# Kernel optimization log

Measured on AMD Instinct MI355X. Metric: run time of the kernel, lower is better.

## Reference

```python
import jax, jax.numpy as jnp
import numpy as np

EMBED_DIM = 1024
NUM_HEADS = 16
HEAD_DIM = EMBED_DIM // NUM_HEADS
R_QKV = 256
R_OUT = 256
B, T = 4, 2048


def setup_inputs() -> dict:
    key = jax.random.key(0)
    k1, k2, k3, k4, k5 = jax.random.split(key, 5)
    s = 0.02
    return {
        "x": jax.random.normal(k1, (B, T, EMBED_DIM), dtype=jnp.float32),
        "W_qkv_v": jax.random.normal(k2, (R_QKV, EMBED_DIM), dtype=jnp.float32) * s,
        "W_qkv_u": jax.random.normal(k3, (3 * EMBED_DIM, R_QKV), dtype=jnp.float32) * s,
        "W_o_v": jax.random.normal(k4, (R_OUT, EMBED_DIM), dtype=jnp.float32) * s,
        "W_o_u": jax.random.normal(k5, (EMBED_DIM, R_OUT), dtype=jnp.float32) * s,
    }


def reference(x, W_qkv_v, W_qkv_u, W_o_v, W_o_u):
    Bq, Tq, C = x.shape
    H, D = NUM_HEADS, HEAD_DIM
    # low-rank qkv projection: x @ V^T @ U^T (torch Linear weight is [out,in])
    qkv = (x @ W_qkv_v.T) @ W_qkv_u.T  # [B,T,3C]
    q, k, v = jnp.split(qkv, 3, axis=-1)
    # split heads -> [B,H,T,D]
    q = q.reshape(Bq, Tq, H, D).transpose(0, 2, 1, 3)
    k = k.reshape(Bq, Tq, H, D).transpose(0, 2, 1, 3)
    v = v.reshape(Bq, Tq, H, D).transpose(0, 2, 1, 3)
    scale = 1.0 / jnp.sqrt(jnp.asarray(D, dtype=x.dtype))
    scores = jnp.einsum('bhtd,bhsd->bhts', q, k) * scale  # [B,H,T,T]
    # softmax in fp32 then cast back, matching torch.softmax(dtype=float32)
    attn = jax.nn.softmax(scores.astype(jnp.float32), axis=-1).astype(q.dtype)
    y = jnp.einsum('bhts,bhsd->bhtd', attn, v)  # [B,H,T,D]
    y = y.transpose(0, 2, 1, 3).reshape(Bq, Tq, C)  # merge heads
    # low-rank output projection
    y = (y @ W_o_v.T) @ W_o_u.T
    return y
```

## Files before the change

kernel.cpp:

```cpp
#include <hip/hip_runtime.h>
#include <hip/hip_bf16.h>

typedef __attribute__((ext_vector_type(8))) short short8;
typedef __attribute__((ext_vector_type(4))) float f32x4;
typedef __attribute__((ext_vector_type(8))) float f32x8;
typedef __attribute__((ext_vector_type(16))) float f32x16;
typedef unsigned short u16;
typedef unsigned int u32;
typedef unsigned long long u64;

__device__ __forceinline__ void gload_lds16(const void* g, void* l) {
  typedef const __attribute__((address_space(1))) u32 gu32;
  typedef __attribute__((address_space(3))) u32 lu32;
  __builtin_amdgcn_global_load_lds((gu32*)g, (lu32*)l, 16, 0, 0);
}

__device__ __forceinline__ u16 f2bf(float f) {
  union { float f; u32 u; } v; v.f = f;
  u32 u = v.u + 0x7FFFu + ((v.u >> 16) & 1u);
  return (u16)(u >> 16);
}

__device__ __forceinline__ u32 cvtpk(float lo, float hiv) {
  u32 r;
  asm("v_cvt_pk_bf16_f32 %0, %1, %2" : "=v"(r) : "v"(lo), "v"(hiv));
  return r;
}

__device__ __forceinline__ void plswap(u32& a, u32& b) {
  asm("v_permlane32_swap_b32 %0, %1" : "+v"(a), "+v"(b));
}

__device__ __forceinline__ float fexp2(float x) {
  float r;
  asm("v_exp_f32 %0, %1" : "=v"(r) : "v"(x));
  return r;
}

__device__ __forceinline__ short8 lds_read8(const u16* base, int byteoff) {
  return *(const short8*)((const char*)base + byteoff);
}

__global__ __launch_bounds__(256) void cast_w_kernel(
    const float* __restrict__ wv, const float* __restrict__ wu,
    const float* __restrict__ wov, const float* __restrict__ wou,
    u16* __restrict__ dst) {
  const long N0 = 262144, N1 = N0 + 786432, N2 = N1 + 262144, N3 = N2 + 262144;
  long i = (long)(blockIdx.x * 256 + threadIdx.x) * 8;
  if (i >= N3) return;
  const float* s;
  if (i < N0) s = wv + i;
  else if (i < N1) s = wu + (i - N0);
  else if (i < N2) s = wov + (i - N1);
  else s = wou + (i - N2);
  float4 a = *(const float4*)s;
  float4 b = *(const float4*)(s + 4);
  short8 o;
  o[0] = (short)f2bf(a.x); o[1] = (short)f2bf(a.y);
  o[2] = (short)f2bf(a.z); o[3] = (short)f2bf(a.w);
  o[4] = (short)f2bf(b.x); o[5] = (short)f2bf(b.y);
  o[6] = (short)f2bf(b.z); o[7] = (short)f2bf(b.w);
  *(short8*)(dst + i) = o;
}

template<int BM, int BN, int MR, int NR, typename OutT, bool VOUT = false>
__global__ __launch_bounds__(256) void gemm_bt(
    OutT* __restrict__ C, const u16* __restrict__ A, const u16* __restrict__ B,
    int N, int K, u16* __restrict__ Vt = nullptr) {
  __shared__ u16 As[BM * 64];
  __shared__ u16 Bs[BN * 64];
  const int tid = threadIdx.x;
  const int l = tid & 63, w = tid >> 6;
  const int wr = w >> 1, wc = w & 1;
  const int bm = blockIdx.y * BM, bn = blockIdx.x * BN;
  const int srow = l >> 3, sslot = (l & 7) ^ srow;

  f32x4 acc[MR][NR] = {};

  const u16* Ag = A + (long)(bm + srow) * K + sslot * 8;
  const u16* Bg = B + (long)(bn + srow) * K + sslot * 8;
  constexpr int CA = BM / 32, CB = BN / 32;

  for (int kt = 0; kt < K; kt += 64) {
#pragma unroll
    for (int c = 0; c < CA; ++c) {
      int ch = w * CA + c;
      gload_lds16(Ag + (long)ch * 8 * K + kt, (char*)As + ch * 1024);
    }
#pragma unroll
    for (int c = 0; c < CB; ++c) {
      int ch = w * CB + c;
      gload_lds16(Bg + (long)ch * 8 * K + kt, (char*)Bs + ch * 1024);
    }
    __syncthreads();
    short8 af[MR][2], bf[NR][2];
#pragma unroll
    for (int i = 0; i < MR; ++i)
#pragma unroll
      for (int kk = 0; kk < 2; ++kk) {
        int row = wr * (MR * 16) + i * 16 + (l & 15);
        af[i][kk] = lds_read8(As, row * 128 + (((kk * 4 + (l >> 4)) ^ (l & 7)) * 16));
      }
#pragma unroll
    for (int j = 0; j < NR; ++j)
#pragma unroll
      for (int kk = 0; kk < 2; ++kk) {
        int col = wc * (NR * 16) + j * 16 + (l & 15);
        bf[j][kk] = lds_read8(Bs, col * 128 + (((kk * 4 + (l >> 4)) ^ (l & 7)) * 16));
      }
#pragma unroll
    for (int kk = 0; kk < 2; ++kk)
#pragma unroll
      for (int i = 0; i < MR; ++i)
#pragma unroll
        for (int j = 0; j < NR; ++j)
          acc[i][j] = __builtin_amdgcn_mfma_f32_16x16x32_bf16(
              af[i][kk], bf[j][kk], acc[i][j], 0, 0, 0);
    __syncthreads();
  }
#pragma unroll
  for (int i = 0; i < MR; ++i)
#pragma unroll
    for (int j = 0; j < NR; ++j) {
      int row = bm + wr * (MR * 16) + i * 16 + (l >> 4) * 4;
      int col = bn + wc * (NR * 16) + j * 16 + (l & 15);
      if (VOUT && col >= 2048) {
        int hh = (col - 2048) >> 6, d = col & 63;
        int bq = row >> 11, tq = row & 2047;
        u64 pk = (u64)f2bf(acc[i][j][0]) | ((u64)f2bf(acc[i][j][1]) << 16) |
                 ((u64)f2bf(acc[i][j][2]) << 32) | ((u64)f2bf(acc[i][j][3]) << 48);
        *(u64*)(Vt + ((long)(bq * 16 + hh) * 64 + d) * 2048 + tq) = pk;
      } else {
#pragma unroll
        for (int r = 0; r < 4; ++r) {
          if constexpr (sizeof(OutT) == 4) {
            C[(long)(row + r) * N + col] = acc[i][j][r];
          } else {
            ((u16*)C)[(long)(row + r) * N + col] = f2bf(acc[i][j][r]);
          }
        }
      }
    }
}

__global__ __launch_bounds__(256) void gemm_a32(
    u16* __restrict__ C, const float* __restrict__ A, const u16* __restrict__ B,
    int N, int K) {
  constexpr int BM = 64, BN = 64, MR = 2, NR = 2;
  __shared__ u16 As[BM * 64];
  __shared__ u16 Bs[BN * 64];
  const int tid = threadIdx.x;
  const int l = tid & 63, w = tid >> 6;
  const int wr = w >> 1, wc = w & 1;
  const int bm = blockIdx.y * BM, bn = blockIdx.x * BN;
  const int srow = l >> 3, sslot = (l & 7) ^ srow;

  f32x4 acc[MR][NR] = {};
  const u16* Bg = B + (long)(bn + srow) * K + sslot * 8;

  for (int kt = 0; kt < K; kt += 64) {
#pragma unroll
    for (int c = 0; c < 2; ++c) {
      int ch = w * 2 + c;
      gload_lds16(Bg + (long)ch * 8 * K + kt, (char*)Bs + ch * 1024);
    }
#pragma unroll
    for (int it = 0; it < 2; ++it) {
      int c = tid + it * 256;
      int row = c >> 3, slot = c & 7;
      const float* src = A + (long)(bm + row) * K + kt + slot * 8;
      float4 a = *(const float4*)src;
      float4 b = *(const float4*)(src + 4);
      union { u32 u[4]; short8 s; } pk;
      pk.u[0] = cvtpk(a.x, a.y);
      pk.u[1] = cvtpk(a.z, a.w);
      pk.u[2] = cvtpk(b.x, b.y);
      pk.u[3] = cvtpk(b.z, b.w);
      *(short8*)((char*)As + row * 128 + ((slot ^ (row & 7)) * 16)) = pk.s;
    }
    __syncthreads();
    short8 af[MR][2], bf[NR][2];
#pragma unroll
    for (int i = 0; i < MR; ++i)
#pragma unroll
      for (int kk = 0; kk < 2; ++kk) {
        int row = wr * (MR * 16) + i * 16 + (l & 15);
        af[i][kk] = lds_read8(As, row * 128 + (((kk * 4 + (l >> 4)) ^ (l & 7)) * 16));
      }
#pragma unroll
    for (int j = 0; j < NR; ++j)
#pragma unroll
      for (int kk = 0; kk < 2; ++kk) {
        int col = wc * (NR * 16) + j * 16 + (l & 15);
        bf[j][kk] = lds_read8(Bs, col * 128 + (((kk * 4 + (l >> 4)) ^ (l & 7)) * 16));
      }
#pragma unroll
    for (int kk = 0; kk < 2; ++kk)
#pragma unroll
      for (int i = 0; i < MR; ++i)
#pragma unroll
        for (int j = 0; j < NR; ++j)
          acc[i][j] = __builtin_amdgcn_mfma_f32_16x16x32_bf16(
              af[i][kk], bf[j][kk], acc[i][j], 0, 0, 0);
    __syncthreads();
  }
#pragma unroll
  for (int i = 0; i < MR; ++i)
#pragma unroll
    for (int j = 0; j < NR; ++j) {
      int row = bm + wr * (MR * 16) + i * 16 + (l >> 4) * 4;
      int col = bn + wc * (NR * 16) + j * 16 + (l & 15);
#pragma unroll
      for (int r = 0; r < 4; ++r)
        C[(long)(row + r) * N + col] = f2bf(acc[i][j][r]);
    }
}

__global__ __launch_bounds__(512, 4) void attn_kernel(
    u16* __restrict__ Y, const u16* __restrict__ QKV, const u16* __restrict__ Vt) {
  constexpr int T = 2048, LDQ = 3072;
  constexpr float SC = 0.18033688011112042f;
  __shared__ u16 SMEM[16384];
  const int tid = threadIdx.x, l = tid & 63, w = tid >> 6;
  const int lq = l & 31, hi = l >> 5;
  const int qt = blockIdx.x, bh = blockIdx.y;
  const int b = bh >> 4, h = bh & 15;
  const long base = (long)b * T * LDQ;
  const int q0 = qt * 256 + w * 32;

  short8 qf[4];
#pragma unroll
  for (int ks = 0; ks < 4; ++ks)
    qf[ks] = *(const short8*)(QKV + base + (long)(q0 + lq) * LDQ + h * 64 +
                              ks * 16 + hi * 8);

  f32x16 o0 = {}, o1 = {};
  float mrow = -3.0e38f, lrow = 0.0f;

  const int c = tid;
  const int kr = c >> 3, ds = (c & 7) ^ (kr & 7);
  const u16* Kg = QKV + base + 1024 + h * 64;
  const u16* Vg = Vt + (long)bh * 64 * T;

  auto STAGE = [&](int kt, int s) {
    u16* Kd = SMEM + s * 8192;
    u16* Vd = Kd + 4096;
    gload_lds16(Kg + (long)(kt + kr) * LDQ + ds * 8, (char*)Kd + c * 16);
    gload_lds16(Vg + (long)kr * T + kt + ds * 8, (char*)Vd + c * 16);
  };

  const int pslA[4] = {((0 + hi) ^ (lq & 7)) * 16, ((2 + hi) ^ (lq & 7)) * 16,
                       ((4 + hi) ^ (lq & 7)) * 16, ((6 + hi) ^ (lq & 7)) * 16};

  auto COMPUTE = [&](const u16* Ks, const u16* Vs) {
    f32x16 p0 = {}, p1 = {};
    __builtin_amdgcn_s_setprio(1);
#pragma unroll
    for (int ks = 0; ks < 4; ++ks) {
      short8 ka = lds_read8(Ks, lq * 128 + pslA[ks]);
      short8 kb = lds_read8(Ks, (32 + lq) * 128 + pslA[ks]);
      p0 = __builtin_amdgcn_mfma_f32_32x32x16_bf16(ka, qf[ks], p0, 0, 0, 0);
      p1 = __builtin_amdgcn_mfma_f32_32x32x16_bf16(kb, qf[ks], p1, 0, 0, 0);
    }
    __builtin_amdgcn_s_setprio(0);
    f32x16 mv = __builtin_elementwise_max(p0, p1);
    f32x8 m8 = __builtin_elementwise_max(
        __builtin_shufflevector(mv, mv, 0, 1, 2, 3, 4, 5, 6, 7),
        __builtin_shufflevector(mv, mv, 8, 9, 10, 11, 12, 13, 14, 15));
    f32x4 m4 = __builtin_elementwise_max(
        __builtin_shufflevector(m8, m8, 0, 1, 2, 3),
        __builtin_shufflevector(m8, m8, 4, 5, 6, 7));
    float mx = fmaxf(fmaxf(m4[0], m4[1]), fmaxf(m4[2], m4[3]));
    mx = fmaxf(mx, __shfl_xor(mx, 32));
    if (!__all(mx - mrow <= 40.0f)) {
      float mnew = fmaxf(mrow, mx);
      float cr = fexp2((mrow - mnew) * SC);
      mrow = mnew;
      lrow *= cr;
      o0 *= cr;
      o1 *= cr;
    }
    float msc = mrow * SC;
    p0 = p0 * SC - msc;
    p1 = p1 * SC - msc;
#pragma unroll
    for (int r = 0; r < 16; ++r) p0[r] = fexp2(p0[r]);
#pragma unroll
    for (int r = 0; r < 16; ++r) p1[r] = fexp2(p1[r]);
    f32x16 sv = p0 + p1;
    f32x8 s8 = __builtin_shufflevector(sv, sv, 0, 1, 2, 3, 4, 5, 6, 7) +
               __builtin_shufflevector(sv, sv, 8, 9, 10, 11, 12, 13, 14, 15);
    f32x4 s4 = __builtin_shufflevector(s8, s8, 0, 1, 2, 3) +
               __builtin_shufflevector(s8, s8, 4, 5, 6, 7);
    float rs = (s4[0] + s4[1]) + (s4[2] + s4[3]);
    rs += __shfl_xor(rs, 32);
    lrow += rs;
    __builtin_amdgcn_s_setprio(1);
#pragma unroll
    for (int ks = 0; ks < 4; ++ks) {
      const f32x16& ps = (ks < 2) ? p0 : p1;
      const int r0 = (ks & 1) * 8;
      u32 uA = cvtpk(ps[r0 + 0], ps[r0 + 1]);
      u32 uB = cvtpk(ps[r0 + 2], ps[r0 + 3]);
      u32 uC = cvtpk(ps[r0 + 4], ps[r0 + 5]);
      u32 uD = cvtpk(ps[r0 + 6], ps[r0 + 7]);
      plswap(uA, uC);
      plswap(uB, uD);
      union { u32 u[4]; short8 s; } pb;
      pb.u[0] = uA; pb.u[1] = uB; pb.u[2] = uC; pb.u[3] = uD;
      short8 va = lds_read8(Vs, lq * 128 + pslA[ks]);
      short8 vb = lds_read8(Vs, (32 + lq) * 128 + pslA[ks]);
      o0 = __builtin_amdgcn_mfma_f32_32x32x16_bf16(va, pb.s, o0, 0, 0, 0);
      o1 = __builtin_amdgcn_mfma_f32_32x32x16_bf16(vb, pb.s, o1, 0, 0, 0);
    }
    __builtin_amdgcn_s_setprio(0);
  };

  STAGE(0, 0);
  __syncthreads();
  for (int t = 0; t < T / 64; ++t) {
    if (t + 1 < T / 64) STAGE((t + 1) * 64, (t + 1) & 1);
    const u16* Ks = SMEM + (t & 1) * 8192;
    COMPUTE(Ks, Ks + 4096);
    __syncthreads();
  }

  float inv = 1.0f / lrow;
  const int row = w * 32 + lq;
#pragma unroll
  for (int df = 0; df < 2; ++df)
#pragma unroll
    for (int r = 0; r < 16; ++r) {
      int d = df * 32 + (r & 3) + 8 * (r >> 2) + 4 * hi;
      float v = (df ? o1[r] : o0[r]) * inv;
      *(u16*)((char*)SMEM + row * 128 + (((d >> 3) ^ (row & 7)) * 16) + (d & 7) * 2) =
          f2bf(v);
    }
  __syncthreads();
#pragma unroll
  for (int it = 0; it < 4; ++it) {
    int cc = tid + it * 512;
    int q = cc >> 3, g = cc & 7;
    int pg = g ^ (q & 7);
    short8 vv = *(const short8*)((const char*)SMEM + q * 128 + pg * 16);
    *(short8*)(Y + (long)(b * T + qt * 256 + q) * 1024 + h * 64 + g * 8) = vv;
  }
}

__global__ void ws_too_small_kernel(float* out) { out[0] = 3.0e38f; }

extern "C" void kernel_launch(void* const* d_in, const int* in_sizes, int n_in,
                              void* d_out, int out_size, void* d_ws, size_t ws_size,
                              hipStream_t stream) {
  (void)in_sizes; (void)n_in; (void)out_size;
  const float* x   = (const float*)d_in[0];
  const float* wv  = (const float*)d_in[1];
  const float* wu  = (const float*)d_in[2];
  const float* wov = (const float*)d_in[3];
  const float* wou = (const float*)d_in[4];
  float* out = (float*)d_out;
  u16* ws = (u16*)d_ws;

  u16* wvb  = ws;
  u16* wub  = ws + 262144;
  u16* wovb = ws + 1048576;
  u16* woub = ws + 1310720;
  u16* t    = ws + 1572864;
  u16* qkv  = ws + 3670016;
  u16* vt   = ws + 28835840;
  u16* yb   = ws + 37224448;
  u16* z    = ws + 45613056;

  if (ws_size < 95420416ull) {
    ws_too_small_kernel<<<1, 1, 0, stream>>>(out);
    return;
  }

  cast_w_kernel<<<dim3(768), dim3(256), 0, stream>>>(wv, wu, wov, wou, ws);
  gemm_a32<<<dim3(4, 128), dim3(256), 0, stream>>>(t, x, wvb, 256, 1024);
  gemm_bt<128, 128, 4, 4, u16, true><<<dim3(24, 64), dim3(256), 0, stream>>>(
      qkv, t, wub, 3072, 256, vt);
  attn_kernel<<<dim3(8, 64), dim3(512), 0, stream>>>(yb, qkv, vt);
  gemm_bt<64, 64, 2, 2, u16><<<dim3(4, 128), dim3(256), 0, stream>>>(z, yb, wovb, 256, 1024);
  gemm_bt<128, 128, 4, 4, float><<<dim3(8, 64), dim3(256), 0, stream>>>(out, z, woub, 1024, 256);
}
```

Measured before the change: 192.2 us.

## Compute softmax row sums via MFMA, defer max rescale, split V transpose kernel

```diff
diff --git a/kernel.cpp b/kernel.cpp
--- a/kernel.cpp
+++ b/kernel.cpp
@@ -3,11 +3,9 @@
 
 typedef __attribute__((ext_vector_type(8))) short short8;
 typedef __attribute__((ext_vector_type(4))) float f32x4;
-typedef __attribute__((ext_vector_type(8))) float f32x8;
 typedef __attribute__((ext_vector_type(16))) float f32x16;
 typedef unsigned short u16;
 typedef unsigned int u32;
-typedef unsigned long long u64;
 
 __device__ __forceinline__ void gload_lds16(const void* g, void* l) {
   typedef const __attribute__((address_space(1))) u32 gu32;
@@ -34,6 +32,12 @@
 __device__ __forceinline__ float fexp2(float x) {
   float r;
   asm("v_exp_f32 %0, %1" : "=v"(r) : "v"(x));
+  return r;
+}
+
+__device__ __forceinline__ float max3f(float a, float b, float c) {
+  float r;
+  asm("v_max3_f32 %0, %1, %2, %3" : "=v"(r) : "v"(a), "v"(b), "v"(c));
   return r;
 }
 
@@ -63,16 +67,16 @@
   *(short8*)(dst + i) = o;
 }
 
-template<int BM, int BN, int MR, int NR, typename OutT, bool VOUT = false>
+template<int BM, int BN, int MR, int NR, typename OutT>
 __global__ __launch_bounds__(256) void gemm_bt(
     OutT* __restrict__ C, const u16* __restrict__ A, const u16* __restrict__ B,
-    int N, int K, u16* __restrict__ Vt = nullptr) {
+    int N, int K) {
   __shared__ u16 As[BM * 64];
   __shared__ u16 Bs[BN * 64];
   const int tid = threadIdx.x;
   const int l = tid & 63, w = tid >> 6;
   const int wr = w >> 1, wc = w & 1;
-  const int bm = blockIdx.y * BM, bn = blockIdx.x * BN;
+  const int bm = blockIdx.x * BM, bn = blockIdx.y * BN;
   const int srow = l >> 3, sslot = (l & 7) ^ srow;
 
   f32x4 acc[MR][NR] = {};
@@ -124,20 +128,12 @@
     for (int j = 0; j < NR; ++j) {
       int row = bm + wr * (MR * 16) + i * 16 + (l >> 4) * 4;
       int col = bn + wc * (NR * 16) + j * 16 + (l & 15);
-      if (VOUT && col >= 2048) {
-        int hh = (col - 2048) >> 6, d = col & 63;
-        int bq = row >> 11, tq = row & 2047;
-        u64 pk = (u64)f2bf(acc[i][j][0]) | ((u64)f2bf(acc[i][j][1]) << 16) |
-                 ((u64)f2bf(acc[i][j][2]) << 32) | ((u64)f2bf(acc[i][j][3]) << 48);
-        *(u64*)(Vt + ((long)(bq * 16 + hh) * 64 + d) * 2048 + tq) = pk;
-      } else {
-#pragma unroll
-        for (int r = 0; r < 4; ++r) {
-          if constexpr (sizeof(OutT) == 4) {
-            C[(long)(row + r) * N + col] = acc[i][j][r];
-          } else {
-            ((u16*)C)[(long)(row + r) * N + col] = f2bf(acc[i][j][r]);
-          }
+#pragma unroll
+      for (int r = 0; r < 4; ++r) {
+        if constexpr (sizeof(OutT) == 4) {
+          C[(long)(row + r) * N + col] = acc[i][j][r];
+        } else {
+          ((u16*)C)[(long)(row + r) * N + col] = f2bf(acc[i][j][r]);
         }
       }
     }
@@ -152,7 +148,7 @@
   const int tid = threadIdx.x;
   const int l = tid & 63, w = tid >> 6;
   const int wr = w >> 1, wc = w & 1;
-  const int bm = blockIdx.y * BM, bn = blockIdx.x * BN;
+  const int bm = blockIdx.x * BM, bn = blockIdx.y * BN;
   const int srow = l >> 3, sslot = (l & 7) ^ srow;
 
   f32x4 acc[MR][NR] = {};
@@ -216,10 +212,38 @@
     }
 }
 
+__global__ __launch_bounds__(256) void vtrans_kernel(
+    u16* __restrict__ Vt, const u16* __restrict__ QKV) {
+  constexpr int T = 2048, LDQ = 3072;
+  __shared__ u16 L[64 * 80];
+  const int tid = threadIdx.x;
+  const int t0 = blockIdx.x * 64, bh = blockIdx.y;
+  const int b = bh >> 4, h = bh & 15;
+  const u16* src = QKV + (long)b * T * LDQ + 2048 + h * 64;
+#pragma unroll
+  for (int it = 0; it < 2; ++it) {
+    int row = (tid >> 3) + it * 32;
+    int d0 = (tid & 7) * 8;
+    short8 v = *(const short8*)(src + (long)(t0 + row) * LDQ + d0);
+#pragma unroll
+    for (int j = 0; j < 8; ++j)
+      L[(d0 + j) * 80 + row] = (u16)(short)v[j];
+  }
+  __syncthreads();
+  u16* dst = Vt + (long)bh * 64 * T + t0;
+#pragma unroll
+  for (int it = 0; it < 2; ++it) {
+    int d = (tid >> 3) + it * 32;
+    int c = (tid & 7) * 8;
+    *(short8*)(dst + (long)d * T + c) = *(const short8*)(&L[d * 80 + c]);
+  }
+}
+
 __global__ __launch_bounds__(512, 4) void attn_kernel(
     u16* __restrict__ Y, const u16* __restrict__ QKV, const u16* __restrict__ Vt) {
   constexpr int T = 2048, LDQ = 3072;
   constexpr float SC = 0.18033688011112042f;
+  constexpr float INV_SC = 5.545177444479562f;
   __shared__ u16 SMEM[16384];
   const int tid = threadIdx.x, l = tid & 63, w = tid >> 6;
   const int lq = l & 31, hi = l >> 5;
@@ -234,8 +258,11 @@
     qf[ks] = *(const short8*)(QKV + base + (long)(q0 + lq) * LDQ + h * 64 +
                               ks * 16 + hi * 8);
 
-  f32x16 o0 = {}, o1 = {};
-  float mrow = -3.0e38f, lrow = 0.0f;
+  const short8 ONES = {(short)0x3F80, (short)0x3F80, (short)0x3F80, (short)0x3F80,
+                       (short)0x3F80, (short)0x3F80, (short)0x3F80, (short)0x3F80};
+
+  f32x16 o0 = {}, o1 = {}, olr = {};
+  float mrow = 0.0f;
 
   const int c = tid;
   const int kr = c >> 3, ds = (c & 7) ^ (kr & 7);
@@ -263,38 +290,36 @@
       p1 = __builtin_amdgcn_mfma_f32_32x32x16_bf16(kb, qf[ks], p1, 0, 0, 0);
     }
     __builtin_amdgcn_s_setprio(0);
-    f32x16 mv = __builtin_elementwise_max(p0, p1);
-    f32x8 m8 = __builtin_elementwise_max(
-        __builtin_shufflevector(mv, mv, 0, 1, 2, 3, 4, 5, 6, 7),
-        __builtin_shufflevector(mv, mv, 8, 9, 10, 11, 12, 13, 14, 15));
-    f32x4 m4 = __builtin_elementwise_max(
-        __builtin_shufflevector(m8, m8, 0, 1, 2, 3),
-        __builtin_shufflevector(m8, m8, 4, 5, 6, 7));
-    float mx = fmaxf(fmaxf(m4[0], m4[1]), fmaxf(m4[2], m4[3]));
-    mx = fmaxf(mx, __shfl_xor(mx, 32));
-    if (!__all(mx - mrow <= 40.0f)) {
-      float mnew = fmaxf(mrow, mx);
-      float cr = fexp2((mrow - mnew) * SC);
-      mrow = mnew;
-      lrow *= cr;
-      o0 *= cr;
-      o1 *= cr;
-    }
     float msc = mrow * SC;
     p0 = p0 * SC - msc;
     p1 = p1 * SC - msc;
+    float a0 = max3f(p0[0], p0[1], p0[2]);
+    float a1 = max3f(p0[3], p0[4], p0[5]);
+    float a2 = max3f(p0[6], p0[7], p0[8]);
+    float a3 = max3f(p0[9], p0[10], p0[11]);
+    float a4 = max3f(p0[12], p0[13], p0[14]);
+    float a5 = max3f(p0[15], p1[0], p1[1]);
+    float a6 = max3f(p1[2], p1[3], p1[4]);
+    float a7 = max3f(p1[5], p1[6], p1[7]);
+    float a8 = max3f(p1[8], p1[9], p1[10]);
+    float a9 = max3f(p1[11], p1[12], p1[13]);
+    float a10 = fmaxf(p1[14], p1[15]);
+    float b0 = max3f(a0, a1, a2);
+    float b1 = max3f(a3, a4, a5);
+    float b2 = max3f(a6, a7, a8);
+    float b3 = fmaxf(a9, a10);
+    float mx = fmaxf(max3f(b0, b1, b2), b3);
+    mx = fmaxf(mx, __shfl_xor(mx, 32));
 #pragma unroll
     for (int r = 0; r < 16; ++r) p0[r] = fexp2(p0[r]);
 #pragma unroll
     for (int r = 0; r < 16; ++r) p1[r] = fexp2(p1[r]);
-    f32x16 sv = p0 + p1;
-    f32x8 s8 = __builtin_shufflevector(sv, sv, 0, 1, 2, 3, 4, 5, 6, 7) +
-               __builtin_shufflevector(sv, sv, 8, 9, 10, 11, 12, 13, 14, 15);
-    f32x4 s4 = __builtin_shufflevector(s8, s8, 0, 1, 2, 3) +
-               __builtin_shufflevector(s8, s8, 4, 5, 6, 7);
-    float rs = (s4[0] + s4[1]) + (s4[2] + s4[3]);
-    rs += __shfl_xor(rs, 32);
-    lrow += rs;
+    if (!__all(mx <= 7.25f)) {
+      float mpos = fmaxf(mx, 0.0f);
+      float cr = fexp2(-mpos);
+      mrow += mpos * INV_SC;
+      p0 *= cr; p1 *= cr; o0 *= cr; o1 *= cr; olr *= cr;
+    }
     __builtin_amdgcn_s_setprio(1);
 #pragma unroll
     for (int ks = 0; ks < 4; ++ks) {
@@ -312,6 +337,7 @@
       short8 vb = lds_read8(Vs, (32 + lq) * 128 + pslA[ks]);
       o0 = __builtin_amdgcn_mfma_f32_32x32x16_bf16(va, pb.s, o0, 0, 0, 0);
       o1 = __builtin_amdgcn_mfma_f32_32x32x16_bf16(vb, pb.s, o1, 0, 0, 0);
+      olr = __builtin_amdgcn_mfma_f32_32x32x16_bf16(ONES, pb.s, olr, 0, 0, 0);
     }
     __builtin_amdgcn_s_setprio(0);
   };
@@ -325,7 +351,7 @@
     __syncthreads();
   }
 
-  float inv = 1.0f / lrow;
+  float inv = 1.0f / olr[0];
   const int row = w * 32 + lq;
 #pragma unroll
   for (int df = 0; df < 2; ++df)
@@ -377,10 +403,10 @@
   }
 
   cast_w_kernel<<<dim3(768), dim3(256), 0, stream>>>(wv, wu, wov, wou, ws);
-  gemm_a32<<<dim3(4, 128), dim3(256), 0, stream>>>(t, x, wvb, 256, 1024);
-  gemm_bt<128, 128, 4, 4, u16, true><<<dim3(24, 64), dim3(256), 0, stream>>>(
-      qkv, t, wub, 3072, 256, vt);
+  gemm_a32<<<dim3(128, 4), dim3(256), 0, stream>>>(t, x, wvb, 256, 1024);
+  gemm_bt<128, 128, 4, 4, u16><<<dim3(64, 24), dim3(256), 0, stream>>>(qkv, t, wub, 3072, 256);
+  vtrans_kernel<<<dim3(32, 64), dim3(256), 0, stream>>>(vt, qkv);
   attn_kernel<<<dim3(8, 64), dim3(512), 0, stream>>>(yb, qkv, vt);
-  gemm_bt<64, 64, 2, 2, u16><<<dim3(4, 128), dim3(256), 0, stream>>>(z, yb, wovb, 256, 1024);
-  gemm_bt<128, 128, 4, 4, float><<<dim3(8, 64), dim3(256), 0, stream>>>(out, z, woub, 1024, 256);
-}
+  gemm_bt<64, 64, 2, 2, u16><<<dim3(128, 4), dim3(256), 0, stream>>>(z, yb, wovb, 256, 1024);
+  gemm_bt<128, 128, 4, 4, float><<<dim3(64, 8), dim3(256), 0, stream>>>(out, z, woub, 1024, 256);
+}
```

New measurement: 173.7 us. 1.11x faster.
